# Kernel optimization log

Hardware: AMD Instinct MI355X
Metric: run time of the kernel (lower is better)

The kernel has to match this reference:

```python
import jax, jax.numpy as jnp
import numpy as np

WIN = (9, 9)
EPS = 1e-05
DN = ('NCHW', 'OIHW', 'NCHW')


def _box_sum(x, win):
    # Separable box-sum (mathematically identical to conv2d with an all-ones
    kh = jnp.ones((1, 1, win[0], 1), x.dtype)
    kw = jnp.ones((1, 1, 1, win[1]), x.dtype)
    ph, pw = win[0] // 2, win[1] // 2
    x = jax.lax.conv_general_dilated(x, kh, (1, 1), [(ph, ph), (0, 0)], dimension_numbers=DN)
    x = jax.lax.conv_general_dilated(x, kw, (1, 1), [(0, 0), (pw, pw)], dimension_numbers=DN)
    return x


def setup_inputs() -> dict:
    key = jax.random.key(0)
    k1, k2 = jax.random.split(key)
    I = jax.random.normal(k1, (16, 1, 1024, 1024), dtype=jnp.float32)
    J = jax.random.normal(k2, (16, 1, 1024, 1024), dtype=jnp.float32)
    return {"I": I, "J": J}


def reference(I, J):
    win_size = WIN[0] * WIN[1]  # 81
    I_sum = _box_sum(I, WIN)
    J_sum = _box_sum(J, WIN)
    I2_sum = _box_sum(I * I, WIN)
    J2_sum = _box_sum(J * J, WIN)
    IJ_sum = _box_sum(I * J, WIN)

    u_I = I_sum / win_size
    u_J = J_sum / win_size

    cross = IJ_sum - u_J * I_sum - u_I * J_sum + u_I * u_J * win_size
    I_var = I2_sum - 2.0 * u_I * I_sum + u_I * u_I * win_size
    J_var = J2_sum - 2.0 * u_J * J_sum + u_J * u_J * win_size

    cc = cross * cross / (I_var * J_var + EPS)
    return -1.0 * jnp.mean(cc) + 1.0
```

## Files before the change

### kernel.cpp

```cpp
#include <hip/hip_runtime.h>

#define W_     1024
#define H_     1024
#define NIMG   16
#define HS     32
#define NTHR   128
#define PAD    4
#define CS_N   (W_ + 2*PAD)
#define EPS_   1e-5f
#define VS_LD  1160

__device__ __forceinline__ int swz(int cs) { return cs + (cs >> 3); }

__global__ __launch_bounds__(NTHR) void ncc_main(const float* __restrict__ Iall,
                                                 const float* __restrict__ Jall,
                                                 float* __restrict__ acc)
{
    const int bx    = blockIdx.x;
    const int img   = bx >> 5;
    const int strip = bx & 31;
    const int r0    = strip * HS;
    const int t     = threadIdx.x;

    const float* __restrict__ Ib = Iall + (size_t)img * (W_ * H_);
    const float* __restrict__ Jb = Jall + (size_t)img * (W_ * H_);

    __shared__ float vs[5][VS_LD];

    if (t < 2 * PAD) {
        int cs = (t < PAD) ? t : (CS_N - 2 * PAD + t);
        #pragma unroll
        for (int ch = 0; ch < 5; ++ch) vs[ch][swz(cs)] = 0.0f;
    }

    float sI[8], sJ[8], sII[8], sJJ[8], sIJ[8];
    #pragma unroll
    for (int k = 0; k < 8; ++k) { sI[k]=0.f; sJ[k]=0.f; sII[k]=0.f; sJJ[k]=0.f; sIJ[k]=0.f; }

    for (int q = r0 - PAD; q < r0 + PAD; ++q) {
        if (q >= 0) {
            #pragma unroll
            for (int k = 0; k < 8; ++k) {
                const int c = t + k * NTHR;
                const float a = Ib[q * W_ + c];
                const float b = Jb[q * W_ + c];
                sI[k]+=a; sJ[k]+=b; sII[k]+=a*a; sJJ[k]+=b*b; sIJ[k]+=a*b;
            }
        }
    }
    __syncthreads();

    float accum = 0.0f;
    const float inv81 = 1.0f / 81.0f;

    for (int r = r0; r < r0 + HS; ++r) {
        const int qe = r + PAD;
        if (qe < H_) {
            #pragma unroll
            for (int k = 0; k < 8; ++k) {
                const int c = t + k * NTHR;
                const float a = Ib[qe * W_ + c];
                const float b = Jb[qe * W_ + c];
                sI[k]+=a; sJ[k]+=b; sII[k]+=a*a; sJJ[k]+=b*b; sIJ[k]+=a*b;
            }
        }
        #pragma unroll
        for (int k = 0; k < 8; ++k) {
            const int idx = swz(t + k * NTHR + PAD);
            vs[0][idx] = sI[k];
            vs[1][idx] = sJ[k];
            vs[2][idx] = sII[k];
            vs[3][idx] = sJJ[k];
            vs[4][idx] = sIJ[k];
        }
        __syncthreads();

        float h[5][8];
        {
            const int base = t * 8;
            #pragma unroll
            for (int ch = 0; ch < 5; ++ch) {
                float w[16];
                #pragma unroll
                for (int x = 0; x < 16; ++x) w[x] = vs[ch][swz(base + x)];
                float s = 0.f;
                #pragma unroll
                for (int x = 0; x < 9; ++x) s += w[x];
                h[ch][0] = s;
                #pragma unroll
                for (int c = 1; c < 8; ++c) { s += w[c + 8] - w[c - 1]; h[ch][c] = s; }
            }
        }
        #pragma unroll
        for (int c = 0; c < 8; ++c) {
            const float SI = h[0][c], SJ = h[1][c];
            const float SII = h[2][c], SJJ = h[3][c], SIJ = h[4][c];
            const float cross = SIJ - SI * SJ * inv81;
            const float iv    = SII - SI * SI * inv81;
            const float jv    = SJJ - SJ * SJ * inv81;
            accum += cross * cross / (iv * jv + EPS_);
        }
        __syncthreads();

        const int ql = r - PAD;
        if (ql >= 0 && r + 1 < r0 + HS) {
            #pragma unroll
            for (int k = 0; k < 8; ++k) {
                const int c = t + k * NTHR;
                const float a = Ib[ql * W_ + c];
                const float b = Jb[ql * W_ + c];
                sI[k]-=a; sJ[k]-=b; sII[k]-=a*a; sJJ[k]-=b*b; sIJ[k]-=a*b;
            }
        }
    }

    #pragma unroll
    for (int off = 32; off > 0; off >>= 1) accum += __shfl_down(accum, off);
    if ((t & 63) == 0) atomicAdd(acc, accum);
}

__global__ void ncc_finalize(const float* __restrict__ acc, float* __restrict__ out)
{
    out[0] = 1.0f - acc[0] * (1.0f / (float)((size_t)NIMG * W_ * H_));
}

extern "C" void kernel_launch(void* const* d_in, const int* in_sizes, int n_in,
                              void* d_out, int out_size, void* d_ws, size_t ws_size,
                              hipStream_t stream)
{
    const float* I = (const float*)d_in[0];
    const float* J = (const float*)d_in[1];
    float* acc = (float*)d_ws;

    hipMemsetAsync(acc, 0, sizeof(float), stream);
    ncc_main<<<NIMG * (H_ / HS), NTHR, 0, stream>>>(I, J, acc);
    ncc_finalize<<<1, 1, 0, stream>>>(acc, (float*)d_out);
}
```

Baseline: 191.0 us.

## Vectorize NCC strip kernel with float4 loads, prefetching, and smaller strips

```diff
diff --git a/kernel.cpp b/kernel.cpp
--- a/kernel.cpp
+++ b/kernel.cpp
@@ -1,117 +1,147 @@
 #include <hip/hip_runtime.h>
 
-#define W_     1024
-#define H_     1024
-#define NIMG   16
-#define HS     32
-#define NTHR   128
-#define PAD    4
-#define CS_N   (W_ + 2*PAD)
-#define EPS_   1e-5f
-#define VS_LD  1160
+#define W_    1024
+#define H_    1024
+#define NIMG  16
+#define HS    16
+#define NTHR  256
+#define PAD   4
+#define EPS_  1e-5f
+#define LDSW  1032
 
-__device__ __forceinline__ int swz(int cs) { return cs + (cs >> 3); }
+__device__ __forceinline__ float4 ldq(const float* p) {
+    return *reinterpret_cast<const float4*>(p);
+}
+__device__ __forceinline__ float4 ldq_or0(const float* p, bool v) {
+    return v ? *reinterpret_cast<const float4*>(p) : make_float4(0.f, 0.f, 0.f, 0.f);
+}
 
-__global__ __launch_bounds__(NTHR) void ncc_main(const float* __restrict__ Iall,
-                                                 const float* __restrict__ Jall,
-                                                 float* __restrict__ acc)
+__global__ __launch_bounds__(NTHR, 4) void ncc_main(const float* __restrict__ Iall,
+                                                    const float* __restrict__ Jall,
+                                                    float* __restrict__ acc)
 {
     const int bx    = blockIdx.x;
-    const int img   = bx >> 5;
-    const int strip = bx & 31;
+    const int sbx   = (bx & 7) * 128 + (bx >> 3);
+    const int img   = sbx >> 6;
+    const int strip = sbx & 63;
     const int r0    = strip * HS;
     const int t     = threadIdx.x;
+    const int c0    = t * 4;
 
-    const float* __restrict__ Ib = Iall + (size_t)img * (W_ * H_);
-    const float* __restrict__ Jb = Jall + (size_t)img * (W_ * H_);
+    const float* __restrict__ Ib = Iall + (size_t)img * (W_ * H_) + c0;
+    const float* __restrict__ Jb = Jall + (size_t)img * (W_ * H_) + c0;
 
-    __shared__ float vs[5][VS_LD];
+    __shared__ float vs[5][LDSW];
 
-    if (t < 2 * PAD) {
-        int cs = (t < PAD) ? t : (CS_N - 2 * PAD + t);
+    if (t < 8) {
+        const int idx = (t < 4) ? t : (1024 + t);
         #pragma unroll
-        for (int ch = 0; ch < 5; ++ch) vs[ch][swz(cs)] = 0.0f;
+        for (int ch = 0; ch < 5; ++ch) vs[ch][idx] = 0.0f;
     }
 
-    float sI[8], sJ[8], sII[8], sJJ[8], sIJ[8];
+    float vsum[5][4];
     #pragma unroll
-    for (int k = 0; k < 8; ++k) { sI[k]=0.f; sJ[k]=0.f; sII[k]=0.f; sJJ[k]=0.f; sIJ[k]=0.f; }
+    for (int ch = 0; ch < 5; ++ch)
+        #pragma unroll
+        for (int k = 0; k < 4; ++k) vsum[ch][k] = 0.f;
 
     for (int q = r0 - PAD; q < r0 + PAD; ++q) {
         if (q >= 0) {
+            const float4 a = ldq(Ib + (size_t)q * W_);
+            const float4 b = ldq(Jb + (size_t)q * W_);
+            const float av[4] = {a.x, a.y, a.z, a.w};
+            const float bv[4] = {b.x, b.y, b.z, b.w};
             #pragma unroll
-            for (int k = 0; k < 8; ++k) {
-                const int c = t + k * NTHR;
-                const float a = Ib[q * W_ + c];
-                const float b = Jb[q * W_ + c];
-                sI[k]+=a; sJ[k]+=b; sII[k]+=a*a; sJJ[k]+=b*b; sIJ[k]+=a*b;
+            for (int k = 0; k < 4; ++k) {
+                vsum[0][k] += av[k];
+                vsum[1][k] += bv[k];
+                vsum[2][k] = __builtin_fmaf(av[k], av[k], vsum[2][k]);
+                vsum[3][k] = __builtin_fmaf(bv[k], bv[k], vsum[3][k]);
+                vsum[4][k] = __builtin_fmaf(av[k], bv[k], vsum[4][k]);
             }
         }
     }
-    __syncthreads();
+
+    float4 eI = ldq_or0(Ib + (size_t)(r0 + PAD) * W_, r0 + PAD < H_);
+    float4 eJ = ldq_or0(Jb + (size_t)(r0 + PAD) * W_, r0 + PAD < H_);
+    float4 lI = ldq_or0(Ib + (size_t)(r0 - PAD) * W_, r0 - PAD >= 0);
+    float4 lJ = ldq_or0(Jb + (size_t)(r0 - PAD) * W_, r0 - PAD >= 0);
 
     float accum = 0.0f;
     const float inv81 = 1.0f / 81.0f;
 
     for (int r = r0; r < r0 + HS; ++r) {
-        const int qe = r + PAD;
-        if (qe < H_) {
+        {
+            const float av[4] = {eI.x, eI.y, eI.z, eI.w};
+            const float bv[4] = {eJ.x, eJ.y, eJ.z, eJ.w};
             #pragma unroll
-            for (int k = 0; k < 8; ++k) {
-                const int c = t + k * NTHR;
-                const float a = Ib[qe * W_ + c];
-                const float b = Jb[qe * W_ + c];
-                sI[k]+=a; sJ[k]+=b; sII[k]+=a*a; sJJ[k]+=b*b; sIJ[k]+=a*b;
+            for (int k = 0; k < 4; ++k) {
+                vsum[0][k] += av[k];
+                vsum[1][k] += bv[k];
+                vsum[2][k] = __builtin_fmaf(av[k], av[k], vsum[2][k]);
+                vsum[3][k] = __builtin_fmaf(bv[k], bv[k], vsum[3][k]);
+                vsum[4][k] = __builtin_fmaf(av[k], bv[k], vsum[4][k]);
             }
         }
         #pragma unroll
-        for (int k = 0; k < 8; ++k) {
-            const int idx = swz(t + k * NTHR + PAD);
-            vs[0][idx] = sI[k];
-            vs[1][idx] = sJ[k];
-            vs[2][idx] = sII[k];
-            vs[3][idx] = sJJ[k];
-            vs[4][idx] = sIJ[k];
+        for (int ch = 0; ch < 5; ++ch)
+            *reinterpret_cast<float4*>(&vs[ch][c0 + 4]) =
+                make_float4(vsum[ch][0], vsum[ch][1], vsum[ch][2], vsum[ch][3]);
+        __syncthreads();
+
+        float4 L[5], R[5];
+        #pragma unroll
+        for (int ch = 0; ch < 5; ++ch) {
+            L[ch] = ldq(&vs[ch][c0]);
+            R[ch] = ldq(&vs[ch][c0 + 8]);
+        }
+
+        const float4 eI2 = ldq_or0(Ib + (size_t)(r + PAD + 1) * W_, r + PAD + 1 < H_);
+        const float4 eJ2 = ldq_or0(Jb + (size_t)(r + PAD + 1) * W_, r + PAD + 1 < H_);
+        const float4 lI2 = ldq_or0(Ib + (size_t)(r - PAD + 1) * W_, r - PAD + 1 >= 0);
+        const float4 lJ2 = ldq_or0(Jb + (size_t)(r - PAD + 1) * W_, r - PAD + 1 >= 0);
+
+        float h[5][4];
+        #pragma unroll
+        for (int ch = 0; ch < 5; ++ch) {
+            float w[12];
+            w[0] = L[ch].x; w[1] = L[ch].y; w[2]  = L[ch].z; w[3]  = L[ch].w;
+            w[4] = vsum[ch][0]; w[5] = vsum[ch][1]; w[6] = vsum[ch][2]; w[7] = vsum[ch][3];
+            w[8] = R[ch].x; w[9] = R[ch].y; w[10] = R[ch].z; w[11] = R[ch].w;
+            float s = w[0];
+            #pragma unroll
+            for (int x = 1; x < 9; ++x) s += w[x];
+            h[ch][0] = s;
+            #pragma unroll
+            for (int c = 1; c < 4; ++c) { s += w[c + 8] - w[c - 1]; h[ch][c] = s; }
+        }
+        #pragma unroll
+        for (int c = 0; c < 4; ++c) {
+            const float SI = h[0][c], SJ = h[1][c];
+            const float SII = h[2][c], SJJ = h[3][c], SIJ = h[4][c];
+            const float cross = __builtin_fmaf(-SI * SJ, inv81, SIJ);
+            const float iv    = __builtin_fmaf(-SI * SI, inv81, SII);
+            const float jv    = __builtin_fmaf(-SJ * SJ, inv81, SJJ);
+            accum = __builtin_fmaf(cross * cross,
+                                   __builtin_amdgcn_rcpf(__builtin_fmaf(iv, jv, EPS_)),
+                                   accum);
+        }
+
+        {
+            const float av[4] = {lI.x, lI.y, lI.z, lI.w};
+            const float bv[4] = {lJ.x, lJ.y, lJ.z, lJ.w};
+            #pragma unroll
+            for (int k = 0; k < 4; ++k) {
+                vsum[0][k] -= av[k];
+                vsum[1][k] -= bv[k];
+                vsum[2][k] = __builtin_fmaf(-av[k], av[k], vsum[2][k]);
+                vsum[3][k] = __builtin_fmaf(-bv[k], bv[k], vsum[3][k]);
+                vsum[4][k] = __builtin_fmaf(-av[k], bv[k], vsum[4][k]);
+            }
         }
         __syncthreads();
 
-        float h[5][8];
-        {
-            const int base = t * 8;
-            #pragma unroll
-            for (int ch = 0; ch < 5; ++ch) {
-                float w[16];
-                #pragma unroll
-                for (int x = 0; x < 16; ++x) w[x] = vs[ch][swz(base + x)];
-                float s = 0.f;
-                #pragma unroll
-                for (int x = 0; x < 9; ++x) s += w[x];
-                h[ch][0] = s;
-                #pragma unroll
-                for (int c = 1; c < 8; ++c) { s += w[c + 8] - w[c - 1]; h[ch][c] = s; }
-            }
-        }
-        #pragma unroll
-        for (int c = 0; c < 8; ++c) {
-            const float SI = h[0][c], SJ = h[1][c];
-            const float SII = h[2][c], SJJ = h[3][c], SIJ = h[4][c];
-            const float cross = SIJ - SI * SJ * inv81;
-            const float iv    = SII - SI * SI * inv81;
-            const float jv    = SJJ - SJ * SJ * inv81;
-            accum += cross * cross / (iv * jv + EPS_);
-        }
-        __syncthreads();
-
-        const int ql = r - PAD;
-        if (ql >= 0 && r + 1 < r0 + HS) {
-            #pragma unroll
-            for (int k = 0; k < 8; ++k) {
-                const int c = t + k * NTHR;
-                const float a = Ib[ql * W_ + c];
-                const float b = Jb[ql * W_ + c];
-                sI[k]-=a; sJ[k]-=b; sII[k]-=a*a; sJJ[k]-=b*b; sIJ[k]-=a*b;
-            }
-        }
+        eI = eI2; eJ = eJ2; lI = lI2; lJ = lJ2;
     }
 
     #pragma unroll
```

Result: slower. 215.1 us (+12.6%).
